# Kernel tuning notes

Hardware: AMD Instinct MI355X
Metric: run time of the kernel (lower is better)

The kernel has to match this reference:

```python
import jax, jax.numpy as jnp
import numpy as np

DIM = 1024
N_HEADS = 16
B, S = 2, 2048


def setup_inputs() -> dict:
    key = jax.random.key(0)
    ks = jax.random.split(key, 5)
    scale = 1.0 / np.sqrt(DIM)
    x = jax.random.normal(ks[0], (B, S, DIM), dtype=jnp.float32)
    mask = jax.random.randint(ks[1], (B, S), 0, 2, dtype=jnp.int32)
    Wq = jax.random.normal(ks[2], (DIM, DIM), dtype=jnp.float32) * scale
    Wk = jax.random.normal(ks[3], (DIM, DIM), dtype=jnp.float32) * scale
    Wv = jax.random.normal(ks[4], (DIM, DIM), dtype=jnp.float32) * scale
    bq = jnp.zeros((DIM,), jnp.float32)
    bk = jnp.zeros((DIM,), jnp.float32)
    bv = jnp.zeros((DIM,), jnp.float32)
    return {"x": x, "mask": mask, "Wq": Wq, "bq": bq, "Wk": Wk, "bk": bk, "Wv": Wv, "bv": bv}


def reference(x, mask, Wq, bq, Wk, bk, Wv, bv):
    # x: (B,S,D); project to q,k,v then split heads: (B,H,S,Dh)
    H = N_HEADS
    Bn, Sn, D = x.shape
    Dh = D // H

    def heads(t):
        return t.reshape(Bn, Sn, H, Dh).transpose(0, 2, 1, 3)

    q = heads(x @ Wq + bq)
    k = heads(x @ Wk + bk)
    v = heads(x @ Wv + bv)

    scores = jnp.einsum("bhsd,bhtd->bhst", q, k) / jnp.sqrt(jnp.float32(Dh))
    m = mask.astype(jnp.float32)[:, None, None, :]  # (B,1,1,S)
    scores = scores - 10000.0 * (1.0 - m)
    attn = jax.nn.softmax(scores, axis=-1)  # dropout is identity at eval (p=0)
    h = jnp.einsum("bhst,bhtd->bhsd", attn, v)
    return h.transpose(0, 2, 1, 3).reshape(Bn, Sn, D)
```

## Files before the change

kernel.cpp:

```cpp
#include <hip/hip_runtime.h>
#include <math.h>

#define DIMD 1024
#define NH 16
#define DH 64
#define BB 2
#define SS 2048
#define M_TOTAL (BB * SS)

typedef _Float16 half8 __attribute__((ext_vector_type(8)));
typedef _Float16 half4v __attribute__((ext_vector_type(4)));
typedef __fp16 fp16x2 __attribute__((ext_vector_type(2)));
typedef float floatx4 __attribute__((ext_vector_type(4)));
typedef float floatx16 __attribute__((ext_vector_type(16)));

#define QSCALE 0.18033688011112042f

__device__ __forceinline__ void load16_to_lds(const void* g, void* l) {
    __builtin_amdgcn_global_load_lds(
        (const __attribute__((address_space(1))) void*)g,
        (__attribute__((address_space(3))) void*)l, 16, 0, 0);
}

__global__ __launch_bounds__(256) void prep_kernel(
    const float* __restrict__ x,
    const float* __restrict__ Wq, const float* __restrict__ Wk,
    const float* __restrict__ Wv, const int* __restrict__ mask,
    _Float16* __restrict__ xh, _Float16* __restrict__ Wt,
    int* __restrict__ pos, int* __restrict__ nvalid)
{
    __shared__ _Float16 Ls[32][34];
    __shared__ int cnt[32], off[32];
    const int bid = blockIdx.x, tid = threadIdx.x;

    if (bid < 1024) {
#pragma unroll
        for (int j = 0; j < 4; ++j) {
            const int i = j * 262144 + bid * 256 + tid;
            float4 v = ((const float4*)x)[i];
            half4v hv = {(_Float16)v.x, (_Float16)v.y, (_Float16)v.z, (_Float16)v.w};
            *(half4v*)&xh[(size_t)i * 4] = hv;
        }
    } else if (bid < 4096) {
        const int wid = bid - 1024;
        const int z = wid >> 10, rem = wid & 1023;
        const float* W = z == 0 ? Wq : (z == 1 ? Wk : Wv);
        _Float16* o = Wt + (size_t)z * DIMD * DIMD;
        const int k0 = (rem >> 5) * 32, n0 = (rem & 31) * 32;
        const int r = tid >> 3, c4 = (tid & 7) * 4;

        float4 v = *(const float4*)&W[(size_t)(k0 + r) * DIMD + n0 + c4];
        Ls[r][c4 + 0] = (_Float16)v.x;
        Ls[r][c4 + 1] = (_Float16)v.y;
        Ls[r][c4 + 2] = (_Float16)v.z;
        Ls[r][c4 + 3] = (_Float16)v.w;
        __syncthreads();
        half4v h = {Ls[c4 + 0][r], Ls[c4 + 1][r], Ls[c4 + 2][r], Ls[c4 + 3][r]};
        *(half4v*)&o[(size_t)(n0 + r) * DIMD + k0 + c4] = h;
    } else {
        const int b = bid - 4096;
        const int wv = tid >> 6, lane = tid & 63;
        const unsigned long long lanemask = (lane == 63)
            ? 0x7fffffffffffffffull : ((1ull << lane) - 1ull);
        unsigned long long bms[8];
#pragma unroll
        for (int cc = 0; cc < 8; ++cc) {
            const int c = wv * 8 + cc;
            const int mv = mask[b * SS + c * 64 + lane];
            bms[cc] = __ballot(mv != 0);
            if (lane == 0) cnt[c] = __popcll(bms[cc]);
        }
        __syncthreads();
        if (tid == 0) {
            int s = 0;
            for (int c = 0; c < 32; ++c) { off[c] = s; s += cnt[c]; }
            nvalid[b] = s;
        }
        __syncthreads();
#pragma unroll
        for (int cc = 0; cc < 8; ++cc) {
            const int c = wv * 8 + cc;
            const int valid = (int)((bms[cc] >> lane) & 1ull);
            pos[b * SS + c * 64 + lane] =
                valid ? (off[c] + __popcll(bms[cc] & lanemask)) : -1;
        }
    }
}

__global__ __launch_bounds__(256) void proj_gemm(
    const _Float16* __restrict__ xh, const _Float16* __restrict__ Wt,
    const float* __restrict__ bq, const float* __restrict__ bk,
    const float* __restrict__ bv, const int* __restrict__ pos,
    _Float16* __restrict__ Q, _Float16* __restrict__ K, _Float16* __restrict__ Vt)
{
    const int z = blockIdx.z;
    const float* bias = z == 0 ? bq : (z == 1 ? bk : bv);
    const _Float16* Wz = Wt + (size_t)z * DIMD * DIMD;

    const _Float16* Aptr; const _Float16* Bptr; int m0, n0;
    if (z == 2) { Aptr = Wz; Bptr = xh; m0 = blockIdx.y * 128; n0 = blockIdx.x * 128; }
    else        { Aptr = xh; Bptr = Wz; m0 = blockIdx.x * 128; n0 = blockIdx.y * 128; }

    __shared__ _Float16 Ah[128 * 64];
    __shared__ _Float16 Bh[128 * 64];

    const int tid = threadIdx.x;
    const int wave = tid >> 6, lane = tid & 63;
    const int quad = lane >> 4, l16 = lane & 15;
    const int wm = (wave >> 1) * 64, wn = (wave & 1) * 64;
    const int sw = l16 & 7;

    floatx4 acc[4][4];
#pragma unroll
    for (int i = 0; i < 4; ++i)
#pragma unroll
        for (int j = 0; j < 4; ++j) acc[i][j] = (floatx4){0.f, 0.f, 0.f, 0.f};

    for (int k0 = 0; k0 < DIMD; k0 += 64) {
        __syncthreads();
#pragma unroll
        for (int it = 0; it < 4; ++it) {
            const int u = it * 256 + tid;
            const int row = u >> 3;
            const int gc = (u & 7) ^ (row & 7);
            load16_to_lds(&Aptr[(size_t)(m0 + row) * DIMD + k0 + gc * 8],
                          &Ah[(size_t)(it * 256 + wave * 64) * 8]);
        }
#pragma unroll
        for (int it = 0; it < 4; ++it) {
            const int u = it * 256 + tid;
            const int row = u >> 3;
            const int gc = (u & 7) ^ (row & 7);
            load16_to_lds(&Bptr[(size_t)(n0 + row) * DIMD + k0 + gc * 8],
                          &Bh[(size_t)(it * 256 + wave * 64) * 8]);
        }
        __syncthreads();

#pragma unroll
        for (int kc = 0; kc < 2; ++kc) {
            const int coff = ((quad + kc * 4) ^ sw) * 8;
            half8 af[4], bf[4];
#pragma unroll
            for (int mt = 0; mt < 4; ++mt)
                af[mt] = *(const half8*)&Ah[(wm + mt * 16 + l16) * 64 + coff];
#pragma unroll
            for (int nt = 0; nt < 4; ++nt)
                bf[nt] = *(const half8*)&Bh[(wn + nt * 16 + l16) * 64 + coff];
#pragma unroll
            for (int mt = 0; mt < 4; ++mt)
#pragma unroll
                for (int nt = 0; nt < 4; ++nt)
                    acc[mt][nt] = __builtin_amdgcn_mfma_f32_16x16x32_f16(
                        af[mt], bf[nt], acc[mt][nt], 0, 0, 0);
        }
    }

    if (z < 2) {
        int prr[4][4];
#pragma unroll
        for (int mt = 0; mt < 4; ++mt)
#pragma unroll
            for (int r = 0; r < 4; ++r) {
                const int m = m0 + wm + mt * 16 + quad * 4 + r;
                prr[mt][r] = (z == 0) ? (m & 2047) : pos[m];
            }
#pragma unroll
        for (int nt = 0; nt < 4; ++nt) {
            const int n = n0 + wn + nt * 16 + l16;
            const float bn = bias[n];
            const int h = n >> 6, d = n & 63;
#pragma unroll
            for (int mt = 0; mt < 4; ++mt) {
#pragma unroll
                for (int r = 0; r < 4; ++r) {
                    if (prr[mt][r] < 0) continue;
                    const int m = m0 + wm + mt * 16 + quad * 4 + r;
                    const int b = m >> 11;
                    const _Float16 val = (_Float16)((acc[mt][nt][r] + bn) *
                                                    (z == 0 ? QSCALE : 1.0f));
                    _Float16* dst = (z == 0) ? Q : K;
                    dst[((((size_t)b * NH + h) * SS + prr[mt][r]) << 6) + d] = val;
                }
            }
        }
    } else {
#pragma unroll
        for (int nt = 0; nt < 4; ++nt) {
            const int gs = n0 + wn + nt * 16 + l16;
            const int prn = pos[gs];
            const int b = gs >> 11;
#pragma unroll
            for (int mt = 0; mt < 4; ++mt) {
#pragma unroll
                for (int r = 0; r < 4; ++r) {
                    if (prn < 0) continue;
                    const int drow = m0 + wm + mt * 16 + quad * 4 + r;
                    const int h = drow >> 6, dh = drow & 63;
                    Vt[(((size_t)b * NH + h) * DH + dh) * SS + prn] =
                        (_Float16)(acc[mt][nt][r] + bias[drow]);
                }
            }
        }
    }
}

__global__ __launch_bounds__(256, 2) void attn_kernel(
    const _Float16* __restrict__ Q, const _Float16* __restrict__ K,
    const _Float16* __restrict__ Vt, const int* __restrict__ nvalid,
    float* __restrict__ out)
{
    __shared__ __align__(16) char smem[34816];
    const int bh = blockIdx.y, b = bh >> 4, h = bh & 15;
    const int q0 = blockIdx.x * 128;
    const int tid = threadIdx.x, wave = tid >> 6, lane = tid & 63;
    const int hi = lane >> 5, l31 = lane & 31;

    const _Float16* Qb = Q + (size_t)bh * SS * DH;
    const _Float16* Kb = K + (size_t)bh * SS * DH;
    const _Float16* Vtb = Vt + (size_t)bh * DH * SS;

    const int nv = nvalid[b];
    const int ntiles = (nv + 63) >> 6;

    half8 qf[4];
#pragma unroll
    for (int ks = 0; ks < 4; ++ks)
        qf[ks] = *(const half8*)&Qb[(size_t)(q0 + wave * 32 + l31) * DH
                                    + ks * 16 + hi * 8];

#pragma unroll
    for (int it = 0; it < 2; ++it) {
        const int u = it * 256 + tid;
        const int row = u >> 3, gc = (u & 7) ^ (row & 7);
        load16_to_lds(&Kb[(size_t)row * DH + gc * 8],
                      (_Float16*)smem + (size_t)(it * 256 + wave * 64) * 8);
    }
#pragma unroll
    for (int it = 0; it < 2; ++it) {
        const int u = it * 256 + tid;
        const int row = u >> 3, gc = (u & 7) ^ (row & 7);
        load16_to_lds(&Vtb[(size_t)row * SS + gc * 8],
                      (_Float16*)(smem + 16384) + (size_t)(it * 256 + wave * 64) * 8);
    }
    __syncthreads();

    floatx16 O0, O1;
#pragma unroll
    for (int r = 0; r < 16; ++r) { O0[r] = 0.f; O1[r] = 0.f; }
    float m = -1e30f, l = 0.f;

    for (int i = 0; i < ntiles; ++i) {
        const int buf = i & 1;
        const int t0 = i * 64;

        if (i + 1 < ntiles) {
            const int nb = buf ^ 1, nt0 = t0 + 64;
            _Float16* KsN = (_Float16*)(smem + nb * 8192);
#pragma unroll
            for (int it = 0; it < 2; ++it) {
                const int u = it * 256 + tid;
                const int row = u >> 3, gc = (u & 7) ^ (row & 7);
                load16_to_lds(&Kb[(size_t)(nt0 + row) * DH + gc * 8],
                              KsN + (size_t)(it * 256 + wave * 64) * 8);
            }
            _Float16* VtN = (_Float16*)(smem + 16384 + nb * 8192);
#pragma unroll
            for (int it = 0; it < 2; ++it) {
                const int u = it * 256 + tid;
                const int row = u >> 3, gc = (u & 7) ^ (row & 7);
                load16_to_lds(&Vtb[(size_t)row * SS + nt0 + gc * 8],
                              VtN + (size_t)(it * 256 + wave * 64) * 8);
            }
        }

        const _Float16* KsB = (const _Float16*)(smem + buf * 8192);
        const _Float16* VtB = (const _Float16*)(smem + 16384 + buf * 8192);

        floatx16 S0, S1;
#pragma unroll
        for (int r = 0; r < 16; ++r) { S0[r] = 0.f; S1[r] = 0.f; }
#pragma unroll
        for (int ks = 0; ks < 4; ++ks) {
            const int c = 2 * ks + hi;
            const int r0 = l31, r1 = 32 + l31;
            half8 a0 = *(const half8*)&KsB[r0 * 64 + ((c ^ (r0 & 7)) << 3)];
            half8 a1 = *(const half8*)&KsB[r1 * 64 + ((c ^ (r1 & 7)) << 3)];
            S0 = __builtin_amdgcn_mfma_f32_32x32x16_f16(a0, qf[ks], S0, 0, 0, 0);
            S1 = __builtin_amdgcn_mfma_f32_32x32x16_f16(a1, qf[ks], S1, 0, 0, 0);
        }

        if (t0 + 64 > nv) {
#pragma unroll
            for (int r = 0; r < 16; ++r) {
                const int tr = (r & 3) + 8 * (r >> 2) + 4 * hi;
                S0[r] = (t0 + tr < nv) ? S0[r] : -1e30f;
                S1[r] = (t0 + 32 + tr < nv) ? S1[r] : -1e30f;
            }
        }

        float tmax = -1e30f;
#pragma unroll
        for (int r = 0; r < 16; ++r)
            tmax = fmaxf(tmax, fmaxf(S0[r], S1[r]));
        tmax = fmaxf(tmax, __shfl_xor(tmax, 32));
        const float mn = fmaxf(m, tmax);
        const float alpha = exp2f(m - mn);
        m = mn;

        float p0[16], p1[16];
        float lsum = 0.f;
#pragma unroll
        for (int r = 0; r < 16; ++r) {
            const float e0 = exp2f(S0[r] - m);
            const float e1 = exp2f(S1[r] - m);
            p0[r] = e0; p1[r] = e1;
            lsum += e0 + e1;
        }
        lsum += __shfl_xor(lsum, 32);
        l = l * alpha + lsum;
#pragma unroll
        for (int r = 0; r < 16; ++r) { O0[r] *= alpha; O1[r] *= alpha; }

        unsigned int pk0[8], pk1[8];
#pragma unroll
        for (int j = 0; j < 8; ++j) {
            union { fp16x2 hv; unsigned int u; } cv;
            cv.hv = __builtin_amdgcn_cvt_pkrtz(p0[2 * j], p0[2 * j + 1]);
            pk0[j] = cv.u;
            cv.hv = __builtin_amdgcn_cvt_pkrtz(p1[2 * j], p1[2 * j + 1]);
            pk1[j] = cv.u;
        }

#pragma unroll
        for (int ks = 0; ks < 4; ++ks) {
            const int k1 = ks & 1;
            const unsigned int* pk = (ks < 2) ? pk0 : pk1;
            const unsigned int a0 = pk[4 * k1 + 0], a1 = pk[4 * k1 + 1];
            const unsigned int b0 = pk[4 * k1 + 2], b1 = pk[4 * k1 + 3];
            const unsigned int s0 = hi ? a0 : b0, s1 = hi ? a1 : b1;
            const unsigned int r0v = __shfl_xor(s0, 32);
            const unsigned int r1v = __shfl_xor(s1, 32);
            union { unsigned int u[4]; half8 hv; } bfu;
            bfu.u[0] = hi ? r0v : a0;
            bfu.u[1] = hi ? r1v : a1;
            bfu.u[2] = hi ? b0 : r0v;
            bfu.u[3] = hi ? b1 : r1v;
            const int c = 2 * ks + hi;
            const int rd0 = l31, rd1 = 32 + l31;
            half8 v0 = *(const half8*)&VtB[rd0 * 64 + ((c ^ (rd0 & 7)) << 3)];
            half8 v1 = *(const half8*)&VtB[rd1 * 64 + ((c ^ (rd1 & 7)) << 3)];
            O0 = __builtin_amdgcn_mfma_f32_32x32x16_f16(v0, bfu.hv, O0, 0, 0, 0);
            O1 = __builtin_amdgcn_mfma_f32_32x32x16_f16(v1, bfu.hv, O1, 0, 0, 0);
        }

        __syncthreads();
    }

    const float inv = 1.f / l;
    float* Ob = (float*)smem + wave * (32 * 68);
#pragma unroll
    for (int r = 0; r < 16; ++r) {
        const int dbase = (r & 3) + 8 * (r >> 2) + 4 * hi;
        Ob[l31 * 68 + dbase] = O0[r] * inv;
        Ob[l31 * 68 + 32 + dbase] = O1[r] * inv;
    }
    __syncthreads();

    const int qq = lane >> 1, part = lane & 1;
    float* op = out + ((size_t)(b * SS + q0 + wave * 32 + qq)) * DIMD
              + h * DH + part * 32;
#pragma unroll
    for (int j = 0; j < 8; ++j)
        *(float4*)&op[j * 4] = *(const float4*)&Ob[qq * 68 + part * 32 + j * 4];
}

extern "C" void kernel_launch(void* const* d_in, const int* in_sizes, int n_in,
                              void* d_out, int out_size, void* d_ws, size_t ws_size,
                              hipStream_t stream) {
    const float* x  = (const float*)d_in[0];
    const int* mask = (const int*)d_in[1];
    const float* Wq = (const float*)d_in[2];
    const float* bq = (const float*)d_in[3];
    const float* Wk = (const float*)d_in[4];
    const float* bk = (const float*)d_in[5];
    const float* Wv = (const float*)d_in[6];
    const float* bv = (const float*)d_in[7];
    float* out = (float*)d_out;

    _Float16* xh = (_Float16*)d_ws;
    _Float16* Wt = xh + (size_t)M_TOTAL * DIMD;
    _Float16* Q  = Wt + (size_t)3 * DIMD * DIMD;
    _Float16* K  = Q + (size_t)M_TOTAL * DIMD;
    _Float16* Vt = K + (size_t)M_TOTAL * DIMD;
    int* pos     = (int*)(Vt + (size_t)M_TOTAL * DIMD);
    int* nvalid  = pos + M_TOTAL;

    prep_kernel<<<4098, 256, 0, stream>>>(x, Wq, Wk, Wv, mask, xh, Wt, pos, nvalid);
    proj_gemm<<<dim3(32, 8, 3), 256, 0, stream>>>(
        xh, Wt, bq, bk, bv, pos, Q, K, Vt);
    attn_kernel<<<dim3(SS / 128, BB * NH), 256, 0, stream>>>(Q, K, Vt, nvalid, out);
}
```

Measured before the change: 183.1 us.

## Fuse fp32-to-fp16 x conversion into projection GEMM with register prefetch

Drops the separate pass that converted x to fp16 and instead has the projection GEMM load fp32 x directly, pack it to fp16 in registers and store it into LDS. The GEMM main loop now prefetches the next k-tile into registers while the current tile is computed, replacing the async global-to-LDS loads and adding a second barrier per iteration. The weight transpose in the prep kernel uses 64x64 tiles with 16-byte stores, and the attention grid is flattened so consecutive blocks map to different heads. This removes an fp16 copy of x and its write/read traffic, but doubles fp32 load bytes inside the GEMM, where x tiles are reread by each of the 8 column blocks, and raises register pressure.

```diff
diff --git a/kernel.cpp b/kernel.cpp
--- a/kernel.cpp
+++ b/kernel.cpp
@@ -22,43 +22,55 @@
         (__attribute__((address_space(3))) void*)l, 16, 0, 0);
 }
 
+__device__ __forceinline__ unsigned pkh(float a, float b) {
+    union { fp16x2 h; unsigned u; } c;
+    c.h = __builtin_amdgcn_cvt_pkrtz(a, b);
+    return c.u;
+}
+__device__ __forceinline__ uint4 pack8(float4 a, float4 b) {
+    uint4 r;
+    r.x = pkh(a.x, a.y); r.y = pkh(a.z, a.w);
+    r.z = pkh(b.x, b.y); r.w = pkh(b.z, b.w);
+    return r;
+}
+
 __global__ __launch_bounds__(256) void prep_kernel(
-    const float* __restrict__ x,
     const float* __restrict__ Wq, const float* __restrict__ Wk,
     const float* __restrict__ Wv, const int* __restrict__ mask,
-    _Float16* __restrict__ xh, _Float16* __restrict__ Wt,
-    int* __restrict__ pos, int* __restrict__ nvalid)
+    _Float16* __restrict__ Wt, int* __restrict__ pos, int* __restrict__ nvalid)
 {
-    __shared__ _Float16 Ls[32][34];
+    __shared__ _Float16 Ls[64][74];
     __shared__ int cnt[32], off[32];
     const int bid = blockIdx.x, tid = threadIdx.x;
 
-    if (bid < 1024) {
-#pragma unroll
-        for (int j = 0; j < 4; ++j) {
-            const int i = j * 262144 + bid * 256 + tid;
-            float4 v = ((const float4*)x)[i];
-            half4v hv = {(_Float16)v.x, (_Float16)v.y, (_Float16)v.z, (_Float16)v.w};
-            *(half4v*)&xh[(size_t)i * 4] = hv;
-        }
-    } else if (bid < 4096) {
-        const int wid = bid - 1024;
-        const int z = wid >> 10, rem = wid & 1023;
+    if (bid < 768) {
+        const int z = bid >> 8, rem = bid & 255;
         const float* W = z == 0 ? Wq : (z == 1 ? Wk : Wv);
         _Float16* o = Wt + (size_t)z * DIMD * DIMD;
-        const int k0 = (rem >> 5) * 32, n0 = (rem & 31) * 32;
-        const int r = tid >> 3, c4 = (tid & 7) * 4;
-
-        float4 v = *(const float4*)&W[(size_t)(k0 + r) * DIMD + n0 + c4];
-        Ls[r][c4 + 0] = (_Float16)v.x;
-        Ls[r][c4 + 1] = (_Float16)v.y;
-        Ls[r][c4 + 2] = (_Float16)v.z;
-        Ls[r][c4 + 3] = (_Float16)v.w;
-        __syncthreads();
-        half4v h = {Ls[c4 + 0][r], Ls[c4 + 1][r], Ls[c4 + 2][r], Ls[c4 + 3][r]};
-        *(half4v*)&o[(size_t)(n0 + r) * DIMD + k0 + c4] = h;
+        const int k0 = (rem >> 4) * 64, n0 = (rem & 15) * 64;
+
+#pragma unroll
+        for (int it = 0; it < 4; ++it) {
+            const int k = it * 16 + (tid >> 4);
+            const int n4 = (tid & 15) * 4;
+            float4 v = *(const float4*)&W[(size_t)(k0 + k) * DIMD + n0 + n4];
+            Ls[k][n4 + 0] = (_Float16)v.x;
+            Ls[k][n4 + 1] = (_Float16)v.y;
+            Ls[k][n4 + 2] = (_Float16)v.z;
+            Ls[k][n4 + 3] = (_Float16)v.w;
+        }
+        __syncthreads();
+#pragma unroll
+        for (int it = 0; it < 2; ++it) {
+            const int idx = it * 256 + tid;
+            const int n = idx >> 3, kc = idx & 7;
+            union { _Float16 h[8]; uint4 u4; } t;
+#pragma unroll
+            for (int j = 0; j < 8; ++j) t.h[j] = Ls[kc * 8 + j][n];
+            *(uint4*)&o[(size_t)(n0 + n) * DIMD + k0 + kc * 8] = t.u4;
+        }
     } else {
-        const int b = bid - 4096;
+        const int b = bid - 768;
         const int wv = tid >> 6, lane = tid & 63;
         const unsigned long long lanemask = (lane == 63)
             ? 0x7fffffffffffffffull : ((1ull << lane) - 1ull);
@@ -88,7 +100,7 @@
 }
 
 __global__ __launch_bounds__(256) void proj_gemm(
-    const _Float16* __restrict__ xh, const _Float16* __restrict__ Wt,
+    const float* __restrict__ x, const _Float16* __restrict__ Wt,
     const float* __restrict__ bq, const float* __restrict__ bk,
     const float* __restrict__ bv, const int* __restrict__ pos,
     _Float16* __restrict__ Q, _Float16* __restrict__ K, _Float16* __restrict__ Vt)
@@ -97,9 +109,9 @@
     const float* bias = z == 0 ? bq : (z == 1 ? bk : bv);
     const _Float16* Wz = Wt + (size_t)z * DIMD * DIMD;
 
-    const _Float16* Aptr; const _Float16* Bptr; int m0, n0;
-    if (z == 2) { Aptr = Wz; Bptr = xh; m0 = blockIdx.y * 128; n0 = blockIdx.x * 128; }
-    else        { Aptr = xh; Bptr = Wz; m0 = blockIdx.x * 128; n0 = blockIdx.y * 128; }
+    int m0, n0;
+    if (z == 2) { m0 = blockIdx.y * 128; n0 = blockIdx.x * 128; }
+    else        { m0 = blockIdx.x * 128; n0 = blockIdx.y * 128; }
 
     __shared__ _Float16 Ah[128 * 64];
     __shared__ _Float16 Bh[128 * 64];
@@ -110,30 +122,56 @@
     const int wm = (wave >> 1) * 64, wn = (wave & 1) * 64;
     const int sw = l16 & 7;
 
+    const int tid8 = tid >> 3;
+    const int gc = (tid & 7) ^ (tid8 & 7);
+    const int xrow0 = (z == 2 ? n0 : m0) + tid8;
+    const int wrow0 = (z == 2 ? m0 : n0) + tid8;
+    const float*    xp = x  + (size_t)xrow0 * DIMD + gc * 8;
+    const _Float16* wp = Wz + (size_t)wrow0 * DIMD + gc * 8;
+    const size_t RS = (size_t)32 * DIMD;
+    _Float16* XW = (z == 2) ? &Bh[(size_t)tid * 8] : &Ah[(size_t)tid * 8];
+    _Float16* WW = (z == 2) ? &Ah[(size_t)tid * 8] : &Bh[(size_t)tid * 8];
+
     floatx4 acc[4][4];
 #pragma unroll
     for (int i = 0; i < 4; ++i)
 #pragma unroll
         for (int j = 0; j < 4; ++j) acc[i][j] = (floatx4){0.f, 0.f, 0.f, 0.f};
 
-    for (int k0 = 0; k0 < DIMD; k0 += 64) {
-        __syncthreads();
-#pragma unroll
-        for (int it = 0; it < 4; ++it) {
-            const int u = it * 256 + tid;
-            const int row = u >> 3;
-            const int gc = (u & 7) ^ (row & 7);
-            load16_to_lds(&Aptr[(size_t)(m0 + row) * DIMD + k0 + gc * 8],
-                          &Ah[(size_t)(it * 256 + wave * 64) * 8]);
-        }
-#pragma unroll
-        for (int it = 0; it < 4; ++it) {
-            const int u = it * 256 + tid;
-            const int row = u >> 3;
-            const int gc = (u & 7) ^ (row & 7);
-            load16_to_lds(&Bptr[(size_t)(n0 + row) * DIMD + k0 + gc * 8],
-                          &Bh[(size_t)(it * 256 + wave * 64) * 8]);
-        }
+    float4 x0, x1, x2, x3, x4, x5, x6, x7;
+    uint4 w0, w1, w2, w3;
+    x0 = *(const float4*)(xp);              x1 = *(const float4*)(xp + 4);
+    x2 = *(const float4*)(xp + RS);         x3 = *(const float4*)(xp + RS + 4);
+    x4 = *(const float4*)(xp + 2 * RS);     x5 = *(const float4*)(xp + 2 * RS + 4);
+    x6 = *(const float4*)(xp + 3 * RS);     x7 = *(const float4*)(xp + 3 * RS + 4);
+    w0 = *(const uint4*)(wp);
+    w1 = *(const uint4*)(wp + RS);
+    w2 = *(const uint4*)(wp + 2 * RS);
+    w3 = *(const uint4*)(wp + 3 * RS);
+
+    for (int kt = 0; kt < 16; ++kt) {
+        *(uint4*)(XW)        = pack8(x0, x1);
+        *(uint4*)(XW + 2048) = pack8(x2, x3);
+        *(uint4*)(XW + 4096) = pack8(x4, x5);
+        *(uint4*)(XW + 6144) = pack8(x6, x7);
+        *(uint4*)(WW)        = w0;
+        *(uint4*)(WW + 2048) = w1;
+        *(uint4*)(WW + 4096) = w2;
+        *(uint4*)(WW + 6144) = w3;
+
+        if (kt < 15) {
+            const float*    xpk = xp + (kt + 1) * 64;
+            const _Float16* wpk = wp + (kt + 1) * 64;
+            x0 = *(const float4*)(xpk);          x1 = *(const float4*)(xpk + 4);
+            x2 = *(const float4*)(xpk + RS);     x3 = *(const float4*)(xpk + RS + 4);
+            x4 = *(const float4*)(xpk + 2 * RS); x5 = *(const float4*)(xpk + 2 * RS + 4);
+            x6 = *(const float4*)(xpk + 3 * RS); x7 = *(const float4*)(xpk + 3 * RS + 4);
+            w0 = *(const uint4*)(wpk);
+            w1 = *(const uint4*)(wpk + RS);
+            w2 = *(const uint4*)(wpk + 2 * RS);
+            w3 = *(const uint4*)(wpk + 3 * RS);
+        }
+
         __syncthreads();
 
 #pragma unroll
@@ -153,6 +191,8 @@
                     acc[mt][nt] = __builtin_amdgcn_mfma_f32_16x16x32_f16(
                         af[mt], bf[nt], acc[mt][nt], 0, 0, 0);
         }
+
+        __syncthreads();
     }
 
     if (z < 2) {
@@ -210,8 +250,11 @@
     float* __restrict__ out)
 {
     __shared__ __align__(16) char smem[34816];
-    const int bh = blockIdx.y, b = bh >> 4, h = bh & 15;
-    const int q0 = blockIdx.x * 128;
+    const int bid = blockIdx.x;
+    const int bh = bid & 31;
+    const int qt = bid >> 5;
+    const int b = bh >> 4, h = bh & 15;
+    const int q0 = qt * 128;
     const int tid = threadIdx.x, wave = tid >> 6, lane = tid & 63;
     const int hi = lane >> 5, l31 = lane & 31;
 
@@ -324,11 +367,8 @@
         unsigned int pk0[8], pk1[8];
 #pragma unroll
         for (int j = 0; j < 8; ++j) {
-            union { fp16x2 hv; unsigned int u; } cv;
-            cv.hv = __builtin_amdgcn_cvt_pkrtz(p0[2 * j], p0[2 * j + 1]);
-            pk0[j] = cv.u;
-            cv.hv = __builtin_amdgcn_cvt_pkrtz(p1[2 * j], p1[2 * j + 1]);
-            pk1[j] = cv.u;
+            pk0[j] = pkh(p0[2 * j], p0[2 * j + 1]);
+            pk1[j] = pkh(p1[2 * j], p1[2 * j + 1]);
         }
 
 #pragma unroll
@@ -387,16 +427,15 @@
     const float* bv = (const float*)d_in[7];
     float* out = (float*)d_out;
 
-    _Float16* xh = (_Float16*)d_ws;
-    _Float16* Wt = xh + (size_t)M_TOTAL * DIMD;
+    _Float16* Wt = (_Float16*)d_ws;
     _Float16* Q  = Wt + (size_t)3 * DIMD * DIMD;
     _Float16* K  = Q + (size_t)M_TOTAL * DIMD;
     _Float16* Vt = K + (size_t)M_TOTAL * DIMD;
     int* pos     = (int*)(Vt + (size_t)M_TOTAL * DIMD);
     int* nvalid  = pos + M_TOTAL;
 
-    prep_kernel<<<4098, 256, 0, stream>>>(x, Wq, Wk, Wv, mask, xh, Wt, pos, nvalid);
+    prep_kernel<<<770, 256, 0, stream>>>(Wq, Wk, Wv, mask, Wt, pos, nvalid);
     proj_gemm<<<dim3(32, 8, 3), 256, 0, stream>>>(
-        xh, Wt, bq, bk, bv, pos, Q, K, Vt);
-    attn_kernel<<<dim3(SS / 128, BB * NH), 256, 0, stream>>>(Q, K, Vt, nvalid, out);
-}
+        x, Wt, bq, bk, bv, pos, Q, K, Vt);
+    attn_kernel<<<512, 256, 0, stream>>>(Q, K, Vt, nvalid, out);
+}
```

Result: no change. 183.4 us (+0.2%).
